# Optimization experiments

Hardware: AMD Instinct MI355X
Metric: run time of the kernel (lower is better)

The kernel has to match this reference:

```python
import jax, jax.numpy as jnp
import numpy as np

N_HEAD = 16
HEAD_DIM = 64


def setup_inputs() -> dict:
    key = jax.random.key(0)
    k1, k2, k3 = jax.random.split(key, 3)
    B, T, C = 1, 4096, 1024
    x = jax.random.normal(k1, (B, T, C), dtype=jnp.float32)
    w_attn = jax.random.normal(k2, (3 * C, C), dtype=jnp.float32) * (C ** -0.5)
    w_proj = jax.random.normal(k3, (C, C), dtype=jnp.float32) * (C ** -0.5)
    return {"x": x, "w_attn": w_attn, "w_proj": w_proj}


def reference(x, w_attn, w_proj):
    B, T, C = x.shape
    H, D = N_HEAD, HEAD_DIM
    qkv = jnp.einsum('btc,fc->btf', x, w_attn)  # [B,T,3C]
    q, k, v = jnp.split(qkv, 3, axis=-1)
    # [B,H,T,D]
    q = q.reshape(B, T, H, D).transpose(0, 2, 1, 3)
    k = k.reshape(B, T, H, D).transpose(0, 2, 1, 3)
    v = v.reshape(B, T, H, D).transpose(0, 2, 1, 3)
    scale = 1.0 / (D ** 0.5)
    att = jnp.einsum('bhqd,bhkd->bhqk', q, k) * scale  # [B,H,T,T]
    causal = jnp.tril(jnp.ones((T, T), dtype=bool))
    att = jnp.where(causal[None, None], att, -jnp.inf)
    att = jax.nn.softmax(att, axis=-1)
    y = jnp.einsum('bhqk,bhkd->bhqd', att, v)  # [B,H,T,D]
    y = y.transpose(0, 2, 1, 3).reshape(B, T, C)
    return jnp.einsum('btc,oc->bto', y, w_proj)
```

## Files before the change

kernel.cpp:

```cpp
#include <hip/hip_runtime.h>

typedef unsigned short u16;
typedef __bf16 bf16x8 __attribute__((ext_vector_type(8)));
typedef float f32x4 __attribute__((ext_vector_type(4)));

__device__ __forceinline__ u16 f2bf(float f) {
  union { float f; unsigned u; } v; v.f = f;
  return (u16)((v.u + 0x7fffu + ((v.u >> 16) & 1u)) >> 16);
}
__device__ __forceinline__ float bf2f(u16 h) {
  union { unsigned u; float f; } v; v.u = ((unsigned)h) << 16;
  return v.f;
}

__device__ __forceinline__ unsigned pkbf(float lo, float hi) {
  union { float f; unsigned u; } a, b; a.f = lo; b.f = hi;
  return __builtin_amdgcn_perm(b.u + 0x8000u, a.u + 0x8000u, 0x07060302u);
}

__device__ __forceinline__ float fexp2(float x) {
#if __has_builtin(__builtin_amdgcn_exp2f)
  return __builtin_amdgcn_exp2f(x);
#else
  return exp2f(x);
#endif
}

__device__ __forceinline__ void gld16(const u16* g, u16* l) {
  __builtin_amdgcn_global_load_lds(
      (const __attribute__((address_space(1))) void*)g,
      (__attribute__((address_space(3))) void*)l, 16, 0, 0);
}


__global__ __launch_bounds__(256) void cvt3(
    const float* __restrict__ x, const float* __restrict__ wa,
    const float* __restrict__ wp, u16* __restrict__ xb,
    u16* __restrict__ wab, u16* __restrict__ wpb)
{
  int b = blockIdx.x;
  const float* in; u16* out; int i;
  if (b < 2048)      { in = x;  out = xb;  i = b * 256 + threadIdx.x; }
  else if (b < 3584) { in = wa; out = wab; i = (b - 2048) * 256 + threadIdx.x; }
  else               { in = wp; out = wpb; i = (b - 3584) * 256 + threadIdx.x; }
  const float* p = in + (size_t)i * 8;
  float4 a = *(const float4*)p, c = *(const float4*)(p + 4);
  uint4 o;
  o.x = pkbf(a.x, a.y); o.y = pkbf(a.z, a.w);
  o.z = pkbf(c.x, c.y); o.w = pkbf(c.z, c.w);
  *(uint4*)&out[(size_t)i * 8] = o;
}

__global__ __launch_bounds__(256) void combine2(
    const u16* __restrict__ O0, const u16* __restrict__ O1,
    const float* __restrict__ l0, const float* __restrict__ l1,
    u16* __restrict__ y)
{
  int i = blockIdx.x * 256 + threadIdx.x;
  int e0 = i * 8;
  int row = e0 >> 10, h = (e0 & 1023) >> 6;
  float inv = 1.0f / (l0[row * 16 + h] + l1[row * 16 + h]);
  uint4 a = *(const uint4*)&O0[(size_t)e0];
  uint4 b = *(const uint4*)&O1[(size_t)e0];
  unsigned aw[4] = {a.x, a.y, a.z, a.w}, bw[4] = {b.x, b.y, b.z, b.w};
  uint4 o;
  unsigned ow[4];
#pragma unroll
  for (int j = 0; j < 4; ++j) {
    float lo = (bf2f((u16)(aw[j] & 0xffffu)) + bf2f((u16)(bw[j] & 0xffffu))) * inv;
    float hi = (bf2f((u16)(aw[j] >> 16))     + bf2f((u16)(bw[j] >> 16)))     * inv;
    ow[j] = pkbf(lo, hi);
  }
  o.x = ow[0]; o.y = ow[1]; o.z = ow[2]; o.w = ow[3];
  *(uint4*)&y[(size_t)e0] = o;
}

template<bool COUT_F32, bool VSPLIT>
__global__ __launch_bounds__(256, 3) void gemm_lds(
    const u16* __restrict__ A, const u16* __restrict__ B, void* __restrict__ C,
    u16* __restrict__ C2, int M, int N, int K, int ldc)
{
  __shared__ u16 S[9216];
  u16* As = S;
  u16* Bs = S + 4096;
  const int tid  = threadIdx.x;
  const int wave = tid >> 6, lane = tid & 63;
  const int quad = lane >> 4, ln = lane & 15;
  const int m0 = blockIdx.y * 128, n0 = blockIdx.x * 128;
  const int wm = (wave >> 1) * 64, wn = (wave & 1) * 64;

  const int srow = wave * 32 + (lane >> 2);
  const int scol = (lane & 3) * 8;

  f32x4 acc[4][4] = {};

  for (int k0 = 0; k0 < K; k0 += 32) {
    __syncthreads();
    const u16* ga = A + (size_t)(m0 + srow) * K + k0 + scol;
    const u16* gb = B + (size_t)(n0 + srow) * K + k0 + scol;
    gld16(ga,                  As + wave * 1024);
    gld16(ga + (size_t)16 * K, As + wave * 1024 + 512);
    gld16(gb,                  Bs + wave * 1024);
    gld16(gb + (size_t)16 * K, Bs + wave * 1024 + 512);
    __syncthreads();

    bf16x8 af[4], bfr[4];
#pragma unroll
    for (int i = 0; i < 4; ++i) af[i]  = *(const bf16x8*)&As[(wm + i * 16 + ln) * 32 + quad * 8];
#pragma unroll
    for (int j = 0; j < 4; ++j) bfr[j] = *(const bf16x8*)&Bs[(wn + j * 16 + ln) * 32 + quad * 8];
#pragma unroll
    for (int i = 0; i < 4; ++i)
#pragma unroll
      for (int j = 0; j < 4; ++j)
        acc[i][j] = __builtin_amdgcn_mfma_f32_16x16x32_bf16(af[i], bfr[j], acc[i][j], 0, 0, 0);
  }

  if constexpr (VSPLIT) {
    if (n0 >= 2048) {
      u16 (*Cs)[72] = (u16(*)[72])S;
      __syncthreads();
#pragma unroll
      for (int c = 0; c < 2; ++c) {
        if ((wave >> 1) == c) {
#pragma unroll
          for (int i = 0; i < 4; ++i)
#pragma unroll
            for (int j = 0; j < 4; ++j)
#pragma unroll
              for (int r = 0; r < 4; ++r) {
                int pos = (i >> 1) * 32 + quad * 8 + (i & 1) * 4 + r;
                Cs[wn + j * 16 + ln][pos] = f2bf(acc[i][j][r]);
              }
        }
        __syncthreads();
        {
          int nl = tid >> 1, mseg = (tid & 1) * 32;
#pragma unroll
          for (int s2 = 0; s2 < 4; ++s2) {
            uint4 v4 = *(const uint4*)&Cs[nl][mseg + s2 * 8];
            *(uint4*)&C2[(size_t)(n0 - 2048 + nl) * 4096 + m0 + c * 64 + mseg + s2 * 8] = v4;
          }
        }
        __syncthreads();
      }
      return;
    }
  }

#pragma unroll
  for (int i = 0; i < 4; ++i)
#pragma unroll
    for (int j = 0; j < 4; ++j)
#pragma unroll
      for (int r = 0; r < 4; ++r) {
        int m = m0 + wm + i * 16 + quad * 4 + r;
        int n = n0 + wn + j * 16 + ln;
        if constexpr (COUT_F32)
          ((float*)C)[(size_t)m * ldc + n] = acc[i][j][r];
        else
          ((u16*)C)[(size_t)m * ldc + n] = f2bf(acc[i][j][r]);
      }
}

template<bool COUT_F32>
__global__ __launch_bounds__(256, 4) void gemm_t64(
    const u16* __restrict__ A, const u16* __restrict__ B, void* __restrict__ C,
    int M, int N, int K, int ldc)
{
  __shared__ u16 S[4096];
  u16* As = S;
  u16* Bs = S + 2048;
  const int tid  = threadIdx.x;
  const int wave = tid >> 6, lane = tid & 63;
  const int quad = lane >> 4, ln = lane & 15;
  const int m0 = blockIdx.y * 64, n0 = blockIdx.x * 64;

  const int srow = wave * 16 + (lane >> 2);
  const int scol = (lane & 3) * 8;

  f32x4 acc[4] = {};

  for (int k0 = 0; k0 < K; k0 += 32) {
    __syncthreads();
    gld16(A + (size_t)(m0 + srow) * K + k0 + scol, As + wave * 512);
    gld16(B + (size_t)(n0 + srow) * K + k0 + scol, Bs + wave * 512);
    __syncthreads();

    bf16x8 af = *(const bf16x8*)&As[(wave * 16 + ln) * 32 + quad * 8];
#pragma unroll
    for (int j = 0; j < 4; ++j) {
      bf16x8 bf = *(const bf16x8*)&Bs[(j * 16 + ln) * 32 + quad * 8];
      acc[j] = __builtin_amdgcn_mfma_f32_16x16x32_bf16(af, bf, acc[j], 0, 0, 0);
    }
  }

#pragma unroll
  for (int j = 0; j < 4; ++j)
#pragma unroll
    for (int r = 0; r < 4; ++r) {
      int m = m0 + wave * 16 + quad * 4 + r;
      int n = n0 + j * 16 + ln;
      if constexpr (COUT_F32)
        ((float*)C)[(size_t)m * ldc + n] = acc[j][r];
      else
        ((u16*)C)[(size_t)m * ldc + n] = f2bf(acc[j][r]);
    }
}

template<bool F32>
__device__ __forceinline__ void stage8(u16* dst, const void* base, size_t off) {
  if constexpr (F32) {
    const float* p = (const float*)base + off;
    float4 a = *(const float4*)p;
    float4 b = *(const float4*)(p + 4);
    uint4 q;
    q.x = pkbf(a.x, a.y); q.y = pkbf(a.z, a.w);
    q.z = pkbf(b.x, b.y); q.w = pkbf(b.z, b.w);
    *(uint4*)dst = q;
  } else {
    *(uint4*)dst = *(const uint4*)((const u16*)base + off);
  }
}

template<bool AF32, bool BF32, bool COUT_F32, bool VSPLIT>
__global__ __launch_bounds__(256) void gemm_bt(
    const void* __restrict__ A, const void* __restrict__ B, void* __restrict__ C,
    u16* __restrict__ C2, int M, int N, int K, int ldc)
{
  __shared__ u16 As[128][40];
  __shared__ u16 Bs[128][40];
  const int tid  = threadIdx.x;
  const int wave = tid >> 6, lane = tid & 63;
  const int quad = lane >> 4, ln = lane & 15;
  const int m0 = blockIdx.y * 128, n0 = blockIdx.x * 128;
  const int wm = (wave >> 1) * 64, wn = (wave & 1) * 64;

  f32x4 acc[4][4] = {};

  for (int k0 = 0; k0 < K; k0 += 32) {
    __syncthreads();
#pragma unroll
    for (int i = 0; i < 2; ++i) {
      int idx = tid + i * 256;
      int row = idx >> 2, seg = (idx & 3) * 8;
      stage8<AF32>(&As[row][seg], A, (size_t)(m0 + row) * K + k0 + seg);
      stage8<BF32>(&Bs[row][seg], B, (size_t)(n0 + row) * K + k0 + seg);
    }
    __syncthreads();
    bf16x8 af[4], bfr[4];
#pragma unroll
    for (int i = 0; i < 4; ++i) af[i]  = *(const bf16x8*)&As[wm + i * 16 + ln][quad * 8];
#pragma unroll
    for (int j = 0; j < 4; ++j) bfr[j] = *(const bf16x8*)&Bs[wn + j * 16 + ln][quad * 8];
#pragma unroll
    for (int i = 0; i < 4; ++i)
#pragma unroll
      for (int j = 0; j < 4; ++j)
        acc[i][j] = __builtin_amdgcn_mfma_f32_16x16x32_bf16(af[i], bfr[j], acc[i][j], 0, 0, 0);
  }

  if constexpr (VSPLIT) {
    if (n0 >= 2048) {
      __shared__ u16 Cs[128][72];
#pragma unroll
      for (int c = 0; c < 2; ++c) {
        if ((wave >> 1) == c) {
#pragma unroll
          for (int i = 0; i < 4; ++i)
#pragma unroll
            for (int j = 0; j < 4; ++j)
#pragma unroll
              for (int r = 0; r < 4; ++r) {
                int pos = (i >> 1) * 32 + quad * 8 + (i & 1) * 4 + r;
                Cs[wn + j * 16 + ln][pos] = f2bf(acc[i][j][r]);
              }
        }
        __syncthreads();
        {
          int nl = tid >> 1, mseg = (tid & 1) * 32;
#pragma unroll
          for (int s2 = 0; s2 < 4; ++s2) {
            uint4 v4 = *(const uint4*)&Cs[nl][mseg + s2 * 8];
            *(uint4*)&C2[(size_t)(n0 - 2048 + nl) * 4096 + m0 + c * 64 + mseg + s2 * 8] = v4;
          }
        }
        __syncthreads();
      }
      return;
    }
  }

#pragma unroll
  for (int i = 0; i < 4; ++i)
#pragma unroll
    for (int j = 0; j < 4; ++j)
#pragma unroll
      for (int r = 0; r < 4; ++r) {
        int m = m0 + wm + i * 16 + quad * 4 + r;
        int n = n0 + wn + j * 16 + ln;
        if constexpr (COUT_F32)
          ((float*)C)[(size_t)m * ldc + n] = acc[i][j][r];
        else
          ((u16*)C)[(size_t)m * ldc + n] = f2bf(acc[i][j][r]);
      }
}

struct StageRegs { uint4 k0, k1, v0, v1; };

__device__ __forceinline__ StageRegs attn_stage_load(
    const u16* __restrict__ qk, const u16* __restrict__ vT,
    int h, int kbase, int tid) {
  StageRegs s;
  {
    int key = tid >> 2, seg = (tid & 3) * 16;
    const u16* kp = qk + (size_t)(kbase + key) * 2048 + 1024 + h * 64 + seg;
    s.k0 = *(const uint4*)kp;
    s.k1 = *(const uint4*)(kp + 8);
  }
  {
    int kh = tid >> 7, d = (tid >> 1) & 63, sg = (tid & 1) * 16;
    const u16* vp = vT + (size_t)(h * 64 + d) * 4096 + kbase + kh * 32 + sg;
    s.v0 = *(const uint4*)vp;
    s.v1 = *(const uint4*)(vp + 8);
  }
  return s;
}

template<bool SPLIT>
__global__ __launch_bounds__(256, SPLIT ? 3 : 2) void attn_fwd(
    const u16* __restrict__ qk, const u16* __restrict__ vT,
    u16* __restrict__ out0, u16* __restrict__ out1,
    float* __restrict__ l0buf, float* __restrict__ l1buf)
{
  __shared__ u16 Ks[2][2][64][40];
  __shared__ u16 Vt[2][2][64][40];

  const int tid  = threadIdx.x;
  const int wave = tid >> 6, lane = tid & 63;
  const int quad = lane >> 4, ln = lane & 15;
  const int bx = blockIdx.x;
  int qt, h, ktb, kte;
  u16* oout; float* lout;
  if constexpr (SPLIT) {
    qt = 31 - (bx >> 5);
    int half = (bx >> 4) & 1;
    h = bx & 15;
    ktb = half ? (qt + 1) : 0;
    kte = half ? (2 * qt + 1) : qt;
    oout = half ? out1 : out0;
    lout = half ? l1buf : l0buf;
  } else {
    qt = (bx < 256) ? (31 - (bx >> 4)) : ((bx - 256) >> 4);
    h = bx & 15;
    ktb = 0; kte = 2 * qt + 1;
    oout = out0; lout = nullptr;
  }
  const float C1 = 0.18033688f;

  const int sq0[2] = { qt * 128 + wave * 32, qt * 128 + wave * 32 + 16 };

  bf16x8 qa[2][2];
#pragma unroll
  for (int s = 0; s < 2; ++s) {
    const u16* qrow = qk + (size_t)(sq0[s] + ln) * 2048 + h * 64;
    qa[s][0] = *(const bf16x8*)(qrow + quad * 8);
    qa[s][1] = *(const bf16x8*)(qrow + 32 + quad * 8);
  }

  f32x4 o[2][4] = {};
  float l_i[2] = {0.f, 0.f};

  StageRegs st = attn_stage_load(qk, vT, h, ktb * 64, tid);
  int b = 0;
  for (int kt = ktb; kt <= kte; ++kt, b ^= 1) {
    {
      int key = tid >> 2, seg = (tid & 3) * 16;
      int kh = seg >> 5, off = seg & 31;
      *(uint4*)&Ks[b][kh][key][off]     = st.k0;
      *(uint4*)&Ks[b][kh][key][off + 8] = st.k1;
      int vh = tid >> 7, d = (tid >> 1) & 63, sg = (tid & 1) * 16;
      *(uint4*)&Vt[b][vh][d][sg]     = st.v0;
      *(uint4*)&Vt[b][vh][d][sg + 8] = st.v1;
    }
    __syncthreads();
    if (kt < kte) st = attn_stage_load(qk, vT, h, (kt + 1) * 64, tid);

    bool act[2];
#pragma unroll
    for (int s = 0; s < 2; ++s) act[s] = (kt * 64 <= sq0[s] + 15);

#pragma unroll 1
    for (int s2 = 0; s2 < 2; ++s2) {
      bf16x8 kf[2][2], vb[4];
#pragma unroll
      for (int hf = 0; hf < 2; ++hf)
#pragma unroll
        for (int tp = 0; tp < 2; ++tp)
          kf[hf][tp] = *(const bf16x8*)&Ks[b][hf][(s2 * 2 + tp) * 16 + ln][quad * 8];
#pragma unroll
      for (int dt = 0; dt < 4; ++dt)
        vb[dt] = *(const bf16x8*)&Vt[b][s2][dt * 16 + ln][quad * 8];

#pragma unroll
      for (int s = 0; s < 2; ++s) {
        if (!act[s]) continue;
        f32x4 sv[2];
#pragma unroll
        for (int tp = 0; tp < 2; ++tp) {
          f32x4 z = {0.f, 0.f, 0.f, 0.f};
          z = __builtin_amdgcn_mfma_f32_16x16x32_bf16(kf[0][tp], qa[s][0], z, 0, 0, 0);
          z = __builtin_amdgcn_mfma_f32_16x16x32_bf16(kf[1][tp], qa[s][1], z, 0, 0, 0);
          sv[tp] = z;
        }
        float p[2][4];
        if (kt * 64 + 63 > sq0[s]) {
          const int qr = sq0[s] + ln;
#pragma unroll
          for (int tp = 0; tp < 2; ++tp) {
            int keyb = kt * 64 + (s2 * 2 + tp) * 16 + quad * 4;
#pragma unroll
            for (int r = 0; r < 4; ++r) {
              float arg = (keyb + r > qr) ? -200.0f : fmaf(sv[tp][r], C1, -46.0f);
              p[tp][r] = fexp2(arg);
            }
          }
        } else {
#pragma unroll
          for (int tp = 0; tp < 2; ++tp)
#pragma unroll
            for (int r = 0; r < 4; ++r)
              p[tp][r] = fexp2(fmaf(sv[tp][r], C1, -46.0f));
        }
        l_i[s] += ((p[0][0] + p[0][1]) + (p[0][2] + p[0][3]))
                + ((p[1][0] + p[1][1]) + (p[1][2] + p[1][3]));
        union { unsigned u[4]; bf16x8 v; } pk;
        pk.u[0] = pkbf(p[0][0], p[0][1]);
        pk.u[1] = pkbf(p[0][2], p[0][3]);
        pk.u[2] = pkbf(p[1][0], p[1][1]);
        pk.u[3] = pkbf(p[1][2], p[1][3]);
#pragma unroll
        for (int dt = 0; dt < 4; ++dt)
          o[s][dt] = __builtin_amdgcn_mfma_f32_16x16x32_bf16(vb[dt], pk.v, o[s][dt], 0, 0, 0);
      }
    }
  }

#pragma unroll
  for (int s = 0; s < 2; ++s) {
    l_i[s] += __shfl_xor(l_i[s], 16);
    l_i[s] += __shfl_xor(l_i[s], 32);
    int rowg = sq0[s] + ln;
    if constexpr (SPLIT) {
#pragma unroll
      for (int dt = 0; dt < 4; ++dt)
#pragma unroll
        for (int r = 0; r < 4; ++r)
          oout[(size_t)rowg * 1024 + h * 64 + dt * 16 + quad * 4 + r] = f2bf(o[s][dt][r]);
      if (quad == 0) lout[rowg * 16 + h] = l_i[s];
    } else {
      float inv = 1.0f / l_i[s];
#pragma unroll
      for (int dt = 0; dt < 4; ++dt)
#pragma unroll
        for (int r = 0; r < 4; ++r)
          oout[(size_t)rowg * 1024 + h * 64 + dt * 16 + quad * 4 + r] = f2bf(o[s][dt][r] * inv);
    }
  }
}

extern "C" void kernel_launch(void* const* d_in, const int* in_sizes, int n_in,
                              void* d_out, int out_size, void* d_ws, size_t ws_size,
                              hipStream_t stream) {
  const float* x      = (const float*)d_in[0];
  const float* w_attn = (const float*)d_in[1];
  const float* w_proj = (const float*)d_in[2];

  char* ws = (char*)d_ws;
  u16* qk = (u16*)ws;
  u16* vT = (u16*)(ws + (16u << 20));

  if (ws_size >= (size_t)(44u << 20)) {
    u16*   wpb = (u16*)(ws + (24u << 20));
    u16*   xb  = (u16*)(ws + (26u << 20));
    u16*   wab = (u16*)(ws + (34u << 20));
    u16*   Op0 = (u16*)(ws + (26u << 20));
    u16*   Op1 = (u16*)(ws + (34u << 20));
    float* l0  = (float*)(ws + (42u << 20));
    float* l1  = (float*)(ws + (42u << 20) + (256u << 10));
    u16*   y   = (u16*)ws;

    cvt3<<<4096, 256, 0, stream>>>(x, w_attn, w_proj, xb, wab, wpb);
    gemm_lds<false, true><<<dim3(24, 32), 256, 0, stream>>>(
        xb, wab, qk, vT, 4096, 3072, 1024, 2048);
    attn_fwd<true><<<dim3(1024), 256, 0, stream>>>(qk, vT, Op0, Op1, l0, l1);
    combine2<<<2048, 256, 0, stream>>>(Op0, Op1, l0, l1, y);
    gemm_t64<true><<<dim3(16, 64), 256, 0, stream>>>(
        y, wpb, d_out, 4096, 1024, 1024, 1024);
  } else if (ws_size >= (size_t)(40u << 20)) {
    u16* wpb = (u16*)(ws + (24u << 20));
    u16* xb  = (u16*)(ws + (26u << 20));
    u16* wab = (u16*)(ws + (34u << 20));
    u16* y   = (u16*)(ws + (26u << 20));

    cvt3<<<4096, 256, 0, stream>>>(x, w_attn, w_proj, xb, wab, wpb);
    gemm_lds<false, true><<<dim3(24, 32), 256, 0, stream>>>(
        xb, wab, qk, vT, 4096, 3072, 1024, 2048);
    attn_fwd<false><<<dim3(512), 256, 0, stream>>>(qk, vT, y, nullptr, nullptr, nullptr);
    gemm_t64<true><<<dim3(16, 64), 256, 0, stream>>>(
        y, wpb, d_out, 4096, 1024, 1024, 1024);
  } else {
    u16* y = (u16*)(ws + (24u << 20));
    gemm_bt<true, true, false, true><<<dim3(24, 32), 256, 0, stream>>>(
        x, w_attn, qk, vT, 4096, 3072, 1024, 2048);
    attn_fwd<false><<<dim3(512), 256, 0, stream>>>(qk, vT, y, nullptr, nullptr, nullptr);
    gemm_bt<false, true, true, false><<<dim3(8, 32), 256, 0, stream>>>(
        y, w_proj, d_out, nullptr, 4096, 1024, 1024, 1024);
  }
}
```

Before: 187.3 us.

## Re-layout attention LDS tiles, compute row sums via MFMA, vectorize output stores

Changes the shared-memory layout of the K and V tiles to [chunk][65][8], so each quad reads a contiguous 16-byte slot with a padded stride, aiming to cut LDS bank conflicts. It replaces the scalar row-sum accumulation and cross-lane shuffles with an extra MFMA against a vector of ones, using the bf16-rounded probabilities. Output stores are packed into 8-byte writes instead of scalar 2-byte stores. The MFMA row sum adds matrix-core work per tile and sums rounded values rather than fp32 ones, and the plain bf16 casts may compile to a different conversion sequence than the old manual packing.

New measurement: 185.9 us. About the same (-0.7%).

```diff
diff --git a/kernel.cpp b/kernel.cpp
--- a/kernel.cpp
+++ b/kernel.cpp
@@ -333,8 +333,8 @@
     u16* __restrict__ out0, u16* __restrict__ out1,
     float* __restrict__ l0buf, float* __restrict__ l1buf)
 {
-  __shared__ u16 Ks[2][2][64][40];
-  __shared__ u16 Vt[2][2][64][40];
+  __shared__ __align__(16) u16 Ks[2][8][65][8];
+  __shared__ __align__(16) u16 Vt[2][8][65][8];
 
   const int tid  = threadIdx.x;
   const int wave = tid >> 6, lane = tid & 63;
@@ -368,20 +368,24 @@
     qa[s][1] = *(const bf16x8*)(qrow + 32 + quad * 8);
   }
 
+  bf16x8 ones;
+#pragma unroll
+  for (int i = 0; i < 8; ++i) ones[i] = (__bf16)1.0f;
+
   f32x4 o[2][4] = {};
-  float l_i[2] = {0.f, 0.f};
+  f32x4 la[2] = {};
 
   StageRegs st = attn_stage_load(qk, vT, h, ktb * 64, tid);
   int b = 0;
   for (int kt = ktb; kt <= kte; ++kt, b ^= 1) {
     {
       int key = tid >> 2, seg = (tid & 3) * 16;
-      int kh = seg >> 5, off = seg & 31;
-      *(uint4*)&Ks[b][kh][key][off]     = st.k0;
-      *(uint4*)&Ks[b][kh][key][off + 8] = st.k1;
-      int vh = tid >> 7, d = (tid >> 1) & 63, sg = (tid & 1) * 16;
-      *(uint4*)&Vt[b][vh][d][sg]     = st.v0;
-      *(uint4*)&Vt[b][vh][d][sg + 8] = st.v1;
+      int hf = seg >> 5, q0 = (seg & 31) >> 3;
+      *(uint4*)&Ks[b][hf * 4 + q0][key][0]     = st.k0;
+      *(uint4*)&Ks[b][hf * 4 + q0 + 1][key][0] = st.k1;
+      int vh = tid >> 7, d = (tid >> 1) & 63, sq = (tid & 1) * 2;
+      *(uint4*)&Vt[b][vh * 4 + sq][d][0]     = st.v0;
+      *(uint4*)&Vt[b][vh * 4 + sq + 1][d][0] = st.v1;
     }
     __syncthreads();
     if (kt < kte) st = attn_stage_load(qk, vT, h, (kt + 1) * 64, tid);
@@ -397,10 +401,10 @@
       for (int hf = 0; hf < 2; ++hf)
 #pragma unroll
         for (int tp = 0; tp < 2; ++tp)
-          kf[hf][tp] = *(const bf16x8*)&Ks[b][hf][(s2 * 2 + tp) * 16 + ln][quad * 8];
+          kf[hf][tp] = *(const bf16x8*)&Ks[b][hf * 4 + quad][(s2 * 2 + tp) * 16 + ln][0];
 #pragma unroll
       for (int dt = 0; dt < 4; ++dt)
-        vb[dt] = *(const bf16x8*)&Vt[b][s2][dt * 16 + ln][quad * 8];
+        vb[dt] = *(const bf16x8*)&Vt[b][s2 * 4 + quad][dt * 16 + ln][0];
 
 #pragma unroll
       for (int s = 0; s < 2; ++s) {
@@ -432,39 +436,41 @@
             for (int r = 0; r < 4; ++r)
               p[tp][r] = fexp2(fmaf(sv[tp][r], C1, -46.0f));
         }
-        l_i[s] += ((p[0][0] + p[0][1]) + (p[0][2] + p[0][3]))
-                + ((p[1][0] + p[1][1]) + (p[1][2] + p[1][3]));
-        union { unsigned u[4]; bf16x8 v; } pk;
-        pk.u[0] = pkbf(p[0][0], p[0][1]);
-        pk.u[1] = pkbf(p[0][2], p[0][3]);
-        pk.u[2] = pkbf(p[1][0], p[1][1]);
-        pk.u[3] = pkbf(p[1][2], p[1][3]);
+        bf16x8 pv;
+        pv[0] = (__bf16)p[0][0]; pv[1] = (__bf16)p[0][1];
+        pv[2] = (__bf16)p[0][2]; pv[3] = (__bf16)p[0][3];
+        pv[4] = (__bf16)p[1][0]; pv[5] = (__bf16)p[1][1];
+        pv[6] = (__bf16)p[1][2]; pv[7] = (__bf16)p[1][3];
+        la[s] = __builtin_amdgcn_mfma_f32_16x16x32_bf16(ones, pv, la[s], 0, 0, 0);
 #pragma unroll
         for (int dt = 0; dt < 4; ++dt)
-          o[s][dt] = __builtin_amdgcn_mfma_f32_16x16x32_bf16(vb[dt], pk.v, o[s][dt], 0, 0, 0);
+          o[s][dt] = __builtin_amdgcn_mfma_f32_16x16x32_bf16(vb[dt], pv, o[s][dt], 0, 0, 0);
       }
     }
   }
 
 #pragma unroll
   for (int s = 0; s < 2; ++s) {
-    l_i[s] += __shfl_xor(l_i[s], 16);
-    l_i[s] += __shfl_xor(l_i[s], 32);
     int rowg = sq0[s] + ln;
+    float l_s = la[s][0];
     if constexpr (SPLIT) {
 #pragma unroll
-      for (int dt = 0; dt < 4; ++dt)
-#pragma unroll
-        for (int r = 0; r < 4; ++r)
-          oout[(size_t)rowg * 1024 + h * 64 + dt * 16 + quad * 4 + r] = f2bf(o[s][dt][r]);
-      if (quad == 0) lout[rowg * 16 + h] = l_i[s];
+      for (int dt = 0; dt < 4; ++dt) {
+        uint2 w;
+        w.x = pkbf(o[s][dt][0], o[s][dt][1]);
+        w.y = pkbf(o[s][dt][2], o[s][dt][3]);
+        *(uint2*)&oout[(size_t)rowg * 1024 + h * 64 + dt * 16 + quad * 4] = w;
+      }
+      if (quad == 0) lout[rowg * 16 + h] = l_s;
     } else {
-      float inv = 1.0f / l_i[s];
-#pragma unroll
-      for (int dt = 0; dt < 4; ++dt)
-#pragma unroll
-        for (int r = 0; r < 4; ++r)
-          oout[(size_t)rowg * 1024 + h * 64 + dt * 16 + quad * 4 + r] = f2bf(o[s][dt][r] * inv);
+      float inv = 1.0f / l_s;
+#pragma unroll
+      for (int dt = 0; dt < 4; ++dt) {
+        uint2 w;
+        w.x = pkbf(o[s][dt][0] * inv, o[s][dt][1] * inv);
+        w.y = pkbf(o[s][dt][2] * inv, o[s][dt][3] * inv);
+        *(uint2*)&oout[(size_t)rowg * 1024 + h * 64 + dt * 16 + quad * 4] = w;
+      }
     }
   }
 }
```
